# Kernel optimization log

Measured on AMD Instinct MI355X. Metric: run time of the kernel, lower is better.

## Reference

```python
import jax, jax.numpy as jnp
import numpy as np

B = 128
NE = 14951   # num entities (FB15k)
NR = 1345    # num relations
D = 200      # complex embedding dim (real+imag concatenated)
NL = 116     # number of numerical literal relations


def setup_inputs() -> dict:
    key = jax.random.key(0)
    ks = jax.random.split(key, 8)
    e1_idx = jax.random.randint(ks[0], (B,), 0, NE)
    r_idx = jax.random.randint(ks[1], (B,), 0, NR)
    E = jax.random.normal(ks[2], (NE, D), dtype=jnp.float32) * 0.1
    R = jax.random.normal(ks[3], (NR, D), dtype=jnp.float32) * 0.1
    nf_weights = jax.random.normal(ks[4], (NR, NL), dtype=jnp.float32) * 0.1
    numerical_literals = jax.random.uniform(ks[5], (NE, NL), dtype=jnp.float32)
    c = jax.random.normal(ks[6], (NL,), dtype=jnp.float32) * 0.1
    var = jax.random.uniform(ks[7], (NL,), dtype=jnp.float32) * 0.5 + 0.1  # positive variances
    return {"e1_idx": e1_idx, "r_idx": r_idx, "E": E, "R": R,
            "nf_weights": nf_weights, "numerical_literals": numerical_literals,
            "c": c, "var": var}


def reference(e1_idx, r_idx, E, R, nf_weights, numerical_literals, c, var):
    d2 = E.shape[1] // 2
    e1 = E[e1_idx]            # [B, D]
    r = R[r_idx]              # [B, D]
    e1_real, e1_img = e1[:, :d2], e1[:, d2:]
    r_real, r_img = r[:, :d2], r[:, d2:]
    E_real, E_img = E[:, :d2], E[:, d2:]

    # ComplEx score against all entities: [B, NE]
    score_l = ((e1_real * r_real) @ E_real.T
               + (e1_real * r_img) @ E_img.T
               + (e1_img * r_real) @ E_img.T
               - (e1_img * r_img) @ E_real.T)

    # KBLN numerical-literal branch
    n_h = numerical_literals[e1_idx]                         # [B, NL]
    n = n_h[:, None, :] - numerical_literals[None, :, :]     # [B, NE, NL]
    phi = jnp.exp(-jnp.square(n - c) / var)                  # RBF, [B, NE, NL]
    w_nf = nf_weights[r_idx]                                 # [B, NL]
    score_n = jnp.einsum('ben,bn->be', phi, w_nf)            # [B, NE]

    return jax.nn.sigmoid(score_l + score_n)
```

## Files before the change

### kernel.cpp

```cpp
#include <hip/hip_runtime.h>

#define B     128
#define NE    14951
#define NEP   14976
#define NR    1345
#define D     200
#define NL    116
#define D2    100
#define EB    4
#define LOG2E 1.4426950408889634f

#define OFF_ET4  0
#define OFF_LT4  (OFF_ET4 + 50*NEP*4)
#define OFF_ST4  (OFF_LT4 + 29*NEP*4)
#define OFF_WB   (OFF_ST4 + 29*NEP*4)
#define OFF_UB   (OFF_WB + 128*200)
#define OFF_FB   (OFF_UB + 128*116)
#define WS_FLOATS (OFF_FB + 128*116)
#define WS_NEEDED ((size_t)WS_FLOATS * 4)

#define NB_A 3042
#define NB_B 1872
#define NB_C 64

__global__ __launch_bounds__(256) void prep_all(
    const int* __restrict__ e1_idx, const int* __restrict__ r_idx,
    const float* __restrict__ E, const float* __restrict__ R,
    const float* __restrict__ nf, const float* __restrict__ lit,
    const float* __restrict__ c, const float* __restrict__ var,
    float* __restrict__ ws)
{
    const int bid = blockIdx.x;
    const int t   = threadIdx.x;

    if (bid < NB_A) {
        const int ebk = bid % 234;
        const int cq  = (bid / 234) * 4 + (t >> 6);
        const int e   = ebk * 64 + (t & 63);
        if (cq >= 50) return;
        float4 v = make_float4(0.f, 0.f, 0.f, 0.f);
        if (e < NE) v = *(const float4*)(E + e*D + 4*cq);
        ((float4*)(ws + OFF_ET4))[cq*NEP + e] = v;
    } else if (bid < NB_A + NB_B) {
        const int idx = bid - NB_A;
        const int ebk = idx % 234;
        const int cq  = (idx / 234) * 4 + (t >> 6);
        const int e   = ebk * 64 + (t & 63);
        if (cq >= 29) return;
        float4 L = make_float4(0.f, 0.f, 0.f, 0.f);
        if (e < NE) L = *(const float4*)(lit + e*NL + 4*cq);
        float4 vv = *(const float4*)(var + 4*cq);
        float4 s;
        s.x = (-LOG2E / vv.x) * L.x * L.x;
        s.y = (-LOG2E / vv.y) * L.y * L.y;
        s.z = (-LOG2E / vv.z) * L.z * L.z;
        s.w = (-LOG2E / vv.w) * L.w * L.w;
        ((float4*)(ws + OFF_LT4))[cq*NEP + e] = L;
        ((float4*)(ws + OFF_ST4))[cq*NEP + e] = s;
    } else {
        const int b  = (bid - NB_A - NB_B) * 2 + (t >> 7);
        const int tt = t & 127;
        const int e1 = e1_idx[b];
        const int r  = r_idx[b];
        float* wb = ws + OFF_WB;
        float* ub = ws + OFF_UB;
        float* fb = ws + OFF_FB;
        if (tt < D2) {
            float e1r = E[e1*D + tt],      e1i = E[e1*D + D2 + tt];
            float rr  = R[r*D + tt],       ri  = R[r*D + D2 + tt];
            wb[b*D + tt]      = e1r*rr - e1i*ri;
            wb[b*D + D2 + tt] = e1r*ri + e1i*rr;
        }
        if (tt < NL) {
            float a = lit[e1*NL + tt] - c[tt];
            float q = -LOG2E / var[tt];
            ub[b*NL + tt] = -2.0f * q * a;
            fb[b*NL + tt] = nf[r*NL + tt] * __builtin_amdgcn_exp2f(q * a * a);
        }
    }
}


#define SL_STEP(pf, cq) do {                                              \
    _Pragma("unroll")                                                     \
    for (int j = 0; j < EB; ++j) {                                        \
        float4 wj = *(const float4*)(wb + (b0+j)*D + 4*(cq));             \
        acc[j] = fmaf(wj.x, (pf).x, acc[j]);                              \
        acc[j] = fmaf(wj.y, (pf).y, acc[j]);                              \
        acc[j] = fmaf(wj.z, (pf).z, acc[j]);                              \
        acc[j] = fmaf(wj.w, (pf).w, acc[j]);                              \
    }                                                                     \
} while (0)

#define SN_STEP(lv, sv, cq) do {                                          \
    _Pragma("unroll")                                                     \
    for (int j = 0; j < EB; ++j) {                                        \
        float4 uj = *(const float4*)(ub + (b0+j)*NL + 4*(cq));            \
        float4 fj = *(const float4*)(fb + (b0+j)*NL + 4*(cq));            \
        acc[j] = fmaf(fj.x, __builtin_amdgcn_exp2f(fmaf(uj.x,(lv).x,(sv).x)), acc[j]); \
        acc[j] = fmaf(fj.y, __builtin_amdgcn_exp2f(fmaf(uj.y,(lv).y,(sv).y)), acc[j]); \
        acc[j] = fmaf(fj.z, __builtin_amdgcn_exp2f(fmaf(uj.z,(lv).z,(sv).z)), acc[j]); \
        acc[j] = fmaf(fj.w, __builtin_amdgcn_exp2f(fmaf(uj.w,(lv).w,(sv).w)), acc[j]); \
    }                                                                     \
} while (0)

__global__ __launch_bounds__(128) void score_kernel(
    const float* __restrict__ et4, const float* __restrict__ lt4,
    const float* __restrict__ st4, const float* __restrict__ wb,
    const float* __restrict__ ub,  const float* __restrict__ fb,
    float* __restrict__ out)
{
    const int lid  = blockIdx.x;
    const int p    = (lid & 7) * 468 + (lid >> 3);
    const int eblk = p >> 5;
    const int bblk = p & 31;
    const int e    = eblk * 128 + threadIdx.x;
    const int b0   = bblk * EB;

    float acc[EB];
#pragma unroll
    for (int j = 0; j < EB; ++j) acc[j] = 0.f;

    const float4* E4 = (const float4*)et4;
    const float4* L4 = (const float4*)lt4;
    const float4* S4 = (const float4*)st4;

    {
        float4 pf0 = E4[0*NEP + e];
        float4 pf1 = E4[1*NEP + e];
        float4 pf2 = E4[2*NEP + e];
        float4 pf3 = E4[3*NEP + e];
        for (int cq0 = 0; cq0 < 48; cq0 += 4) {
            SL_STEP(pf0, cq0 + 0); pf0 = E4[min(cq0 + 4, 49)*NEP + e];
            SL_STEP(pf1, cq0 + 1); pf1 = E4[min(cq0 + 5, 49)*NEP + e];
            SL_STEP(pf2, cq0 + 2); pf2 = E4[min(cq0 + 6, 49)*NEP + e];
            SL_STEP(pf3, cq0 + 3); pf3 = E4[min(cq0 + 7, 49)*NEP + e];
        }
        SL_STEP(pf0, 48);
        SL_STEP(pf1, 49);
    }

    {
        float4 lv0 = L4[0*NEP + e], sv0 = S4[0*NEP + e];
        float4 lv1 = L4[1*NEP + e], sv1 = S4[1*NEP + e];
        float4 lv2 = L4[2*NEP + e], sv2 = S4[2*NEP + e];
        float4 lv3 = L4[3*NEP + e], sv3 = S4[3*NEP + e];
        for (int cq0 = 0; cq0 < 28; cq0 += 4) {
            SN_STEP(lv0, sv0, cq0 + 0);
            lv0 = L4[min(cq0 + 4, 28)*NEP + e]; sv0 = S4[min(cq0 + 4, 28)*NEP + e];
            SN_STEP(lv1, sv1, cq0 + 1);
            lv1 = L4[min(cq0 + 5, 28)*NEP + e]; sv1 = S4[min(cq0 + 5, 28)*NEP + e];
            SN_STEP(lv2, sv2, cq0 + 2);
            lv2 = L4[min(cq0 + 6, 28)*NEP + e]; sv2 = S4[min(cq0 + 6, 28)*NEP + e];
            SN_STEP(lv3, sv3, cq0 + 3);
            lv3 = L4[min(cq0 + 7, 28)*NEP + e]; sv3 = S4[min(cq0 + 7, 28)*NEP + e];
        }
        SN_STEP(lv0, sv0, 28);
    }

    if (e < NE) {
#pragma unroll
        for (int j = 0; j < EB; ++j) {
            float s = __builtin_amdgcn_rcpf(1.0f + __builtin_amdgcn_exp2f(acc[j] * -LOG2E));
            out[(b0+j)*NE + e] = s;
        }
    }
}


#define ET  4
#define OFF_W   0
#define OFF_A   25600
#define OFF_WNF 40448
#define OFF_NQ  55296

__global__ __launch_bounds__(128) void prep_kernel_legacy(
    const int* __restrict__ e1_idx, const int* __restrict__ r_idx,
    const float* __restrict__ E, const float* __restrict__ R,
    const float* __restrict__ nf, const float* __restrict__ lit,
    const float* __restrict__ c, const float* __restrict__ var,
    float* __restrict__ ws)
{
    const int b = blockIdx.x;
    const int t = threadIdx.x;
    const int e1 = e1_idx[b];
    const int r  = r_idx[b];
    if (t < D2) {
        float e1r = E[e1*D + t], e1i = E[e1*D + D2 + t];
        float rr  = R[r*D + t],  ri  = R[r*D + D2 + t];
        ws[OFF_W + (t >> 2)*512        + (b << 2) + (t & 3)] = e1r*rr - e1i*ri;
        ws[OFF_W + ((t >> 2) + 25)*512 + (b << 2) + (t & 3)] = e1r*ri + e1i*rr;
    }
    if (t < NL) {
        ws[OFF_A   + (t >> 2)*512 + (b << 2) + (t & 3)] = lit[e1*NL + t] - c[t];
        ws[OFF_WNF + (t >> 2)*512 + (b << 2) + (t & 3)] = nf[r*NL + t];
        if (b == 0) ws[OFF_NQ + t] = -LOG2E / var[t];
    }
}

__global__ __launch_bounds__(128) void main_kernel_legacy(
    const float* __restrict__ E, const float* __restrict__ lit,
    const float* __restrict__ ws, float* __restrict__ out)
{
    const int b  = threadIdx.x;
    const int e0 = blockIdx.x * ET;
    const float4* w4   = (const float4*)(ws + OFF_W);
    const float4* a4   = (const float4*)(ws + OFF_A);
    const float4* wnf4 = (const float4*)(ws + OFF_WNF);
    const float*  nq   = ws + OFF_NQ;
    int eidx[ET];
#pragma unroll
    for (int j = 0; j < ET; ++j) eidx[j] = min(e0 + j, NE - 1);
    float acc[ET];
#pragma unroll
    for (int j = 0; j < ET; ++j) acc[j] = 0.0f;
    for (int dc = 0; dc < D; dc += 4) {
        float4 wv = w4[(dc >> 2)*B + b];
#pragma unroll
        for (int j = 0; j < ET; ++j) {
            float4 ev = *(const float4*)(E + eidx[j]*D + dc);
            acc[j] = fmaf(wv.x, ev.x, acc[j]);
            acc[j] = fmaf(wv.y, ev.y, acc[j]);
            acc[j] = fmaf(wv.z, ev.z, acc[j]);
            acc[j] = fmaf(wv.w, ev.w, acc[j]);
        }
    }
    for (int lc = 0; lc < NL; lc += 4) {
        float4 av = a4[(lc >> 2)*B + b];
        float4 wv = wnf4[(lc >> 2)*B + b];
        float4 q  = *(const float4*)(nq + lc);
#pragma unroll
        for (int j = 0; j < ET; ++j) {
            float4 lv = *(const float4*)(lit + eidx[j]*NL + lc);
            float t0 = av.x - lv.x, t1 = av.y - lv.y, t2 = av.z - lv.z, t3 = av.w - lv.w;
            acc[j] += wv.x * __builtin_amdgcn_exp2f(t0*t0*q.x);
            acc[j] += wv.y * __builtin_amdgcn_exp2f(t1*t1*q.y);
            acc[j] += wv.z * __builtin_amdgcn_exp2f(t2*t2*q.z);
            acc[j] += wv.w * __builtin_amdgcn_exp2f(t3*t3*q.w);
        }
    }
#pragma unroll
    for (int j = 0; j < ET; ++j) {
        float s = 1.0f / (1.0f + __builtin_amdgcn_exp2f(acc[j] * -LOG2E));
        int e = e0 + j;
        if (e < NE) out[b*NE + e] = s;
    }
}


extern "C" void kernel_launch(void* const* d_in, const int* in_sizes, int n_in,
                              void* d_out, int out_size, void* d_ws, size_t ws_size,
                              hipStream_t stream) {
    const int*   e1_idx = (const int*)d_in[0];
    const int*   r_idx  = (const int*)d_in[1];
    const float* E      = (const float*)d_in[2];
    const float* R      = (const float*)d_in[3];
    const float* nf     = (const float*)d_in[4];
    const float* lit    = (const float*)d_in[5];
    const float* c      = (const float*)d_in[6];
    const float* var    = (const float*)d_in[7];
    float* out = (float*)d_out;
    float* ws  = (float*)d_ws;

    if (ws_size >= WS_NEEDED) {
        prep_all<<<NB_A + NB_B + NB_C, 256, 0, stream>>>(
            e1_idx, r_idx, E, R, nf, lit, c, var, ws);
        score_kernel<<<117 * 32, 128, 0, stream>>>(
            ws + OFF_ET4, ws + OFF_LT4, ws + OFF_ST4,
            ws + OFF_WB, ws + OFF_UB, ws + OFF_FB, out);
    } else {
        prep_kernel_legacy<<<B, 128, 0, stream>>>(e1_idx, r_idx, E, R, nf, lit, c, var, ws);
        main_kernel_legacy<<<(NE + ET - 1)/ET, B, 0, stream>>>(E, lit, ws, out);
    }
}
```

Measured before the change: 62.30 us.

## Store transposed entity and literal tables as bf16, recompute literal square term

The prep pass now packs the transposed entity embeddings and numerical literals into bf16 (round-to-nearest-even) instead of fp32, which halves their workspace footprint. The score kernel widens them back to fp32 with shifts. The precomputed per-entity squared-literal table is dropped and recomputed in the score kernel from the bf16 literal and a per-column coefficient. The aim is to cut the global-memory traffic of both the prep writes and the score-kernel reads, at the cost of bf16 rounding error in scores and a little extra ALU work.

```diff
diff --git a/kernel.cpp b/kernel.cpp
--- a/kernel.cpp
+++ b/kernel.cpp
@@ -10,16 +10,24 @@
 #define EB    4
 #define LOG2E 1.4426950408889634f
 
-#define OFF_ET4  0
-#define OFF_LT4  (OFF_ET4 + 50*NEP*4)
-#define OFF_ST4  (OFF_LT4 + 29*NEP*4)
-#define OFF_WB   (OFF_ST4 + 29*NEP*4)
+#define OFF_ET8  0
+#define OFF_LT4  (OFF_ET8 + 25*NEP*4)
+#define OFF_WB   (OFF_LT4 + 29*NEP*2)
 #define OFF_UB   (OFF_WB + 128*200)
 #define OFF_FB   (OFF_UB + 128*116)
-#define WS_FLOATS (OFF_FB + 128*116)
+#define OFF_NQ   (OFF_FB + 128*116)
+#define WS_FLOATS (OFF_NQ + 128)
 #define WS_NEEDED ((size_t)WS_FLOATS * 4)
 
-#define NB_A 3042
+__device__ __forceinline__ unsigned bf16rne(float f) {
+    unsigned u = __float_as_uint(f);
+    u += 0x7FFFu + ((u >> 16) & 1u);
+    return u >> 16;
+}
+#define BF2F_LO(u) __uint_as_float((u) << 16)
+#define BF2F_HI(u) __uint_as_float((u) & 0xffff0000u)
+
+#define NB_A 1638
 #define NB_B 1872
 #define NB_C 64
 
@@ -37,26 +45,30 @@
         const int ebk = bid % 234;
         const int cq  = (bid / 234) * 4 + (t >> 6);
         const int e   = ebk * 64 + (t & 63);
-        if (cq >= 50) return;
-        float4 v = make_float4(0.f, 0.f, 0.f, 0.f);
-        if (e < NE) v = *(const float4*)(E + e*D + 4*cq);
-        ((float4*)(ws + OFF_ET4))[cq*NEP + e] = v;
+        if (cq >= 25) return;
+        uint4 o = make_uint4(0u, 0u, 0u, 0u);
+        if (e < NE) {
+            float4 a = *(const float4*)(E + e*D + 8*cq);
+            float4 b = *(const float4*)(E + e*D + 8*cq + 4);
+            o.x = bf16rne(a.x) | (bf16rne(a.y) << 16);
+            o.y = bf16rne(a.z) | (bf16rne(a.w) << 16);
+            o.z = bf16rne(b.x) | (bf16rne(b.y) << 16);
+            o.w = bf16rne(b.z) | (bf16rne(b.w) << 16);
+        }
+        ((uint4*)(ws + OFF_ET8))[cq*NEP + e] = o;
     } else if (bid < NB_A + NB_B) {
         const int idx = bid - NB_A;
         const int ebk = idx % 234;
         const int cq  = (idx / 234) * 4 + (t >> 6);
         const int e   = ebk * 64 + (t & 63);
         if (cq >= 29) return;
-        float4 L = make_float4(0.f, 0.f, 0.f, 0.f);
-        if (e < NE) L = *(const float4*)(lit + e*NL + 4*cq);
-        float4 vv = *(const float4*)(var + 4*cq);
-        float4 s;
-        s.x = (-LOG2E / vv.x) * L.x * L.x;
-        s.y = (-LOG2E / vv.y) * L.y * L.y;
-        s.z = (-LOG2E / vv.z) * L.z * L.z;
-        s.w = (-LOG2E / vv.w) * L.w * L.w;
-        ((float4*)(ws + OFF_LT4))[cq*NEP + e] = L;
-        ((float4*)(ws + OFF_ST4))[cq*NEP + e] = s;
+        uint2 o = make_uint2(0u, 0u);
+        if (e < NE) {
+            float4 L = *(const float4*)(lit + e*NL + 4*cq);
+            o.x = bf16rne(L.x) | (bf16rne(L.y) << 16);
+            o.y = bf16rne(L.z) | (bf16rne(L.w) << 16);
+        }
+        ((uint2*)(ws + OFF_LT4))[cq*NEP + e] = o;
     } else {
         const int b  = (bid - NB_A - NB_B) * 2 + (t >> 7);
         const int tt = t & 127;
@@ -76,38 +88,53 @@
             float q = -LOG2E / var[tt];
             ub[b*NL + tt] = -2.0f * q * a;
             fb[b*NL + tt] = nf[r*NL + tt] * __builtin_amdgcn_exp2f(q * a * a);
+            if (b == 0) ws[OFF_NQ + tt] = q;
         }
     }
 }
 
 
 #define SL_STEP(pf, cq) do {                                              \
+    float e0f = BF2F_LO((pf).x), e1f = BF2F_HI((pf).x);                   \
+    float e2f = BF2F_LO((pf).y), e3f = BF2F_HI((pf).y);                   \
+    float e4f = BF2F_LO((pf).z), e5f = BF2F_HI((pf).z);                   \
+    float e6f = BF2F_LO((pf).w), e7f = BF2F_HI((pf).w);                   \
     _Pragma("unroll")                                                     \
     for (int j = 0; j < EB; ++j) {                                        \
-        float4 wj = *(const float4*)(wb + (b0+j)*D + 4*(cq));             \
-        acc[j] = fmaf(wj.x, (pf).x, acc[j]);                              \
-        acc[j] = fmaf(wj.y, (pf).y, acc[j]);                              \
-        acc[j] = fmaf(wj.z, (pf).z, acc[j]);                              \
-        acc[j] = fmaf(wj.w, (pf).w, acc[j]);                              \
+        float4 wa = *(const float4*)(wb + (b0+j)*D + 8*(cq));             \
+        float4 wc = *(const float4*)(wb + (b0+j)*D + 8*(cq) + 4);         \
+        acc[j] = fmaf(wa.x, e0f, acc[j]);                                 \
+        acc[j] = fmaf(wa.y, e1f, acc[j]);                                 \
+        acc[j] = fmaf(wa.z, e2f, acc[j]);                                 \
+        acc[j] = fmaf(wa.w, e3f, acc[j]);                                 \
+        acc[j] = fmaf(wc.x, e4f, acc[j]);                                 \
+        acc[j] = fmaf(wc.y, e5f, acc[j]);                                 \
+        acc[j] = fmaf(wc.z, e6f, acc[j]);                                 \
+        acc[j] = fmaf(wc.w, e7f, acc[j]);                                 \
     }                                                                     \
 } while (0)
 
-#define SN_STEP(lv, sv, cq) do {                                          \
+#define SN_STEP(lv, cq) do {                                              \
+    float L0 = BF2F_LO((lv).x), L1 = BF2F_HI((lv).x);                     \
+    float L2 = BF2F_LO((lv).y), L3 = BF2F_HI((lv).y);                     \
+    float4 q = *(const float4*)(nq + 4*(cq));                             \
+    float s0 = (q.x*L0)*L0, s1 = (q.y*L1)*L1;                             \
+    float s2 = (q.z*L2)*L2, s3 = (q.w*L3)*L3;                             \
     _Pragma("unroll")                                                     \
     for (int j = 0; j < EB; ++j) {                                        \
         float4 uj = *(const float4*)(ub + (b0+j)*NL + 4*(cq));            \
         float4 fj = *(const float4*)(fb + (b0+j)*NL + 4*(cq));            \
-        acc[j] = fmaf(fj.x, __builtin_amdgcn_exp2f(fmaf(uj.x,(lv).x,(sv).x)), acc[j]); \
-        acc[j] = fmaf(fj.y, __builtin_amdgcn_exp2f(fmaf(uj.y,(lv).y,(sv).y)), acc[j]); \
-        acc[j] = fmaf(fj.z, __builtin_amdgcn_exp2f(fmaf(uj.z,(lv).z,(sv).z)), acc[j]); \
-        acc[j] = fmaf(fj.w, __builtin_amdgcn_exp2f(fmaf(uj.w,(lv).w,(sv).w)), acc[j]); \
+        acc[j] = fmaf(fj.x, __builtin_amdgcn_exp2f(fmaf(uj.x, L0, s0)), acc[j]); \
+        acc[j] = fmaf(fj.y, __builtin_amdgcn_exp2f(fmaf(uj.y, L1, s1)), acc[j]); \
+        acc[j] = fmaf(fj.z, __builtin_amdgcn_exp2f(fmaf(uj.z, L2, s2)), acc[j]); \
+        acc[j] = fmaf(fj.w, __builtin_amdgcn_exp2f(fmaf(uj.w, L3, s3)), acc[j]); \
     }                                                                     \
 } while (0)
 
 __global__ __launch_bounds__(128) void score_kernel(
-    const float* __restrict__ et4, const float* __restrict__ lt4,
-    const float* __restrict__ st4, const float* __restrict__ wb,
-    const float* __restrict__ ub,  const float* __restrict__ fb,
+    const float* __restrict__ et8, const float* __restrict__ lt4,
+    const float* __restrict__ wb,  const float* __restrict__ ub,
+    const float* __restrict__ fb,  const float* __restrict__ nq,
     float* __restrict__ out)
 {
     const int lid  = blockIdx.x;
@@ -121,41 +148,43 @@
 #pragma unroll
     for (int j = 0; j < EB; ++j) acc[j] = 0.f;
 
-    const float4* E4 = (const float4*)et4;
-    const float4* L4 = (const float4*)lt4;
-    const float4* S4 = (const float4*)st4;
+    const uint4* E4 = (const uint4*)et8;
+    const uint2* L4 = (const uint2*)lt4;
 
     {
-        float4 pf0 = E4[0*NEP + e];
-        float4 pf1 = E4[1*NEP + e];
-        float4 pf2 = E4[2*NEP + e];
-        float4 pf3 = E4[3*NEP + e];
-        for (int cq0 = 0; cq0 < 48; cq0 += 4) {
-            SL_STEP(pf0, cq0 + 0); pf0 = E4[min(cq0 + 4, 49)*NEP + e];
-            SL_STEP(pf1, cq0 + 1); pf1 = E4[min(cq0 + 5, 49)*NEP + e];
-            SL_STEP(pf2, cq0 + 2); pf2 = E4[min(cq0 + 6, 49)*NEP + e];
-            SL_STEP(pf3, cq0 + 3); pf3 = E4[min(cq0 + 7, 49)*NEP + e];
-        }
-        SL_STEP(pf0, 48);
-        SL_STEP(pf1, 49);
+        uint4 pf0 = E4[0*NEP + e];
+        uint4 pf1 = E4[1*NEP + e];
+        uint4 pf2 = E4[2*NEP + e];
+        uint4 pf3 = E4[3*NEP + e];
+        for (int cq0 = 0; cq0 < 20; cq0 += 4) {
+            SL_STEP(pf0, cq0 + 0); pf0 = E4[(cq0 + 4)*NEP + e];
+            SL_STEP(pf1, cq0 + 1); pf1 = E4[(cq0 + 5)*NEP + e];
+            SL_STEP(pf2, cq0 + 2); pf2 = E4[(cq0 + 6)*NEP + e];
+            SL_STEP(pf3, cq0 + 3); pf3 = E4[(cq0 + 7)*NEP + e];
+        }
+        SL_STEP(pf0, 20); pf0 = E4[24*NEP + e];
+        SL_STEP(pf1, 21);
+        SL_STEP(pf2, 22);
+        SL_STEP(pf3, 23);
+        SL_STEP(pf0, 24);
     }
 
     {
-        float4 lv0 = L4[0*NEP + e], sv0 = S4[0*NEP + e];
-        float4 lv1 = L4[1*NEP + e], sv1 = S4[1*NEP + e];
-        float4 lv2 = L4[2*NEP + e], sv2 = S4[2*NEP + e];
-        float4 lv3 = L4[3*NEP + e], sv3 = S4[3*NEP + e];
-        for (int cq0 = 0; cq0 < 28; cq0 += 4) {
-            SN_STEP(lv0, sv0, cq0 + 0);
-            lv0 = L4[min(cq0 + 4, 28)*NEP + e]; sv0 = S4[min(cq0 + 4, 28)*NEP + e];
-            SN_STEP(lv1, sv1, cq0 + 1);
-            lv1 = L4[min(cq0 + 5, 28)*NEP + e]; sv1 = S4[min(cq0 + 5, 28)*NEP + e];
-            SN_STEP(lv2, sv2, cq0 + 2);
-            lv2 = L4[min(cq0 + 6, 28)*NEP + e]; sv2 = S4[min(cq0 + 6, 28)*NEP + e];
-            SN_STEP(lv3, sv3, cq0 + 3);
-            lv3 = L4[min(cq0 + 7, 28)*NEP + e]; sv3 = S4[min(cq0 + 7, 28)*NEP + e];
-        }
-        SN_STEP(lv0, sv0, 28);
+        uint2 lv0 = L4[0*NEP + e];
+        uint2 lv1 = L4[1*NEP + e];
+        uint2 lv2 = L4[2*NEP + e];
+        uint2 lv3 = L4[3*NEP + e];
+        for (int cq0 = 0; cq0 < 24; cq0 += 4) {
+            SN_STEP(lv0, cq0 + 0); lv0 = L4[(cq0 + 4)*NEP + e];
+            SN_STEP(lv1, cq0 + 1); lv1 = L4[(cq0 + 5)*NEP + e];
+            SN_STEP(lv2, cq0 + 2); lv2 = L4[(cq0 + 6)*NEP + e];
+            SN_STEP(lv3, cq0 + 3); lv3 = L4[(cq0 + 7)*NEP + e];
+        }
+        SN_STEP(lv0, 24); lv0 = L4[28*NEP + e];
+        SN_STEP(lv1, 25);
+        SN_STEP(lv2, 26);
+        SN_STEP(lv3, 27);
+        SN_STEP(lv0, 28);
     }
 
     if (e < NE) {
@@ -172,7 +201,7 @@
 #define OFF_W   0
 #define OFF_A   25600
 #define OFF_WNF 40448
-#define OFF_NQ  55296
+#define OFF_NQL 55296
 
 __global__ __launch_bounds__(128) void prep_kernel_legacy(
     const int* __restrict__ e1_idx, const int* __restrict__ r_idx,
@@ -194,7 +223,7 @@
     if (t < NL) {
         ws[OFF_A   + (t >> 2)*512 + (b << 2) + (t & 3)] = lit[e1*NL + t] - c[t];
         ws[OFF_WNF + (t >> 2)*512 + (b << 2) + (t & 3)] = nf[r*NL + t];
-        if (b == 0) ws[OFF_NQ + t] = -LOG2E / var[t];
+        if (b == 0) ws[OFF_NQL + t] = -LOG2E / var[t];
     }
 }
 
@@ -207,7 +236,7 @@
     const float4* w4   = (const float4*)(ws + OFF_W);
     const float4* a4   = (const float4*)(ws + OFF_A);
     const float4* wnf4 = (const float4*)(ws + OFF_WNF);
-    const float*  nq   = ws + OFF_NQ;
+    const float*  nqv  = ws + OFF_NQL;
     int eidx[ET];
 #pragma unroll
     for (int j = 0; j < ET; ++j) eidx[j] = min(e0 + j, NE - 1);
@@ -228,7 +257,7 @@
     for (int lc = 0; lc < NL; lc += 4) {
         float4 av = a4[(lc >> 2)*B + b];
         float4 wv = wnf4[(lc >> 2)*B + b];
-        float4 q  = *(const float4*)(nq + lc);
+        float4 q  = *(const float4*)(nqv + lc);
 #pragma unroll
         for (int j = 0; j < ET; ++j) {
             float4 lv = *(const float4*)(lit + eidx[j]*NL + lc);
@@ -266,8 +295,8 @@
         prep_all<<<NB_A + NB_B + NB_C, 256, 0, stream>>>(
             e1_idx, r_idx, E, R, nf, lit, c, var, ws);
         score_kernel<<<117 * 32, 128, 0, stream>>>(
-            ws + OFF_ET4, ws + OFF_LT4, ws + OFF_ST4,
-            ws + OFF_WB, ws + OFF_UB, ws + OFF_FB, out);
+            ws + OFF_ET8, ws + OFF_LT4,
+            ws + OFF_WB, ws + OFF_UB, ws + OFF_FB, ws + OFF_NQ, out);
     } else {
         prep_kernel_legacy<<<B, 128, 0, stream>>>(e1_idx, r_idx, E, R, nf, lit, c, var, ws);
         main_kernel_legacy<<<(NE + ET - 1)/ET, B, 0, stream>>>(E, lit, ws, out);
```

Result: slower. 63.90 us (+2.6%).
